# Optimization experiments

Hardware: AMD Instinct MI355X
Metric: run time of the kernel (lower is better)

Reference implementation:

```python
import jax, jax.numpy as jnp
import numpy as np

B, N, K = 32, 1024, 20

def _knn_idx(x, k):
    # x: [B, N, C] -> indices of k nearest neighbors (excluding self): [B, N, k]
    sq = jnp.sum(x * x, axis=-1)                      # [B, N]
    d = sq[:, :, None] + sq[:, None, :] - 2.0 * jnp.einsum('bnc,bmc->bnm', x, x)
    d = jnp.where(jnp.eye(x.shape[1], dtype=bool)[None], jnp.inf, d)
    _, idx = jax.lax.top_k(-d, k)                     # smallest distances
    return idx

def _edge_conv(x, k, mlp):
    # x: [B, N, C]; dynamic kNN graph + nn(cat[x_i, x_j - x_i]) + max over neighbors
    idx = _knn_idx(x, k)                              # [B, N, k]
    xj = jax.vmap(lambda xb, ib: xb[ib])(x, idx)      # [B, N, k, C]
    xi = jnp.broadcast_to(x[:, :, None, :], xj.shape)
    msg = mlp(jnp.concatenate([xi, xj - xi], axis=-1))  # [B, N, k, H]
    return jnp.max(msg, axis=2)                       # [B, N, H]

def setup_inputs() -> dict:
    key = jax.random.key(0)
    ks = jax.random.split(key, 16)
    def lin(kk, fi, fo):
        return jax.random.normal(kk, (fi, fo), dtype=jnp.float32) / np.sqrt(fi)
    x = jax.random.normal(ks[0], (B * N, 3), dtype=jnp.float32)
    batch = jnp.repeat(jnp.arange(B, dtype=jnp.int64), N)
    return {
        'x': x, 'batch': batch,
        'W1': lin(ks[1], 6, 64),   'b1': jnp.zeros((64,), jnp.float32),
        'W2': lin(ks[2], 64, 64),  'b2': jnp.zeros((64,), jnp.float32),
        'W3': lin(ks[3], 64, 64),  'b3': jnp.zeros((64,), jnp.float32),
        'W4': lin(ks[4], 128, 128),'b4': jnp.zeros((128,), jnp.float32),
        'Wp': lin(ks[5], 128, 512),'bp': jnp.zeros((512,), jnp.float32),
        'Wt1': lin(ks[6], 512, 256),'bt1': jnp.zeros((256,), jnp.float32),
        'Wt2': lin(ks[7], 256, 40), 'bt2': jnp.zeros((40,), jnp.float32),
    }

def reference(x, batch, W1, b1, W2, b2, W3, b3, W4, b4, Wp, bp, Wt1, bt1, Wt2, bt2):
    xb = x.reshape(B, N, -1)  # equal-sized clouds per batch vector
    mlp1 = lambda h: jax.nn.relu(jax.nn.relu(jax.nn.relu(h @ W1 + b1) @ W2 + b2) @ W3 + b3)
    mlp2 = lambda h: jax.nn.relu(h @ W4 + b4)
    out = _edge_conv(xb, K, mlp1)          # [B, N, 64]
    out = _edge_conv(out, K, mlp2)         # [B, N, 128]
    out = jax.nn.relu(out @ Wp + bp)       # [B, N, 512]
    out = jnp.max(out, axis=1)             # global max pool -> [B, 512]
    out = jax.nn.relu(out @ Wt1 + bt1) @ Wt2 + bt2  # [B, 40]
    return out
```

## Files before the change

### kernel.cpp

```cpp
#include <hip/hip_runtime.h>
#include <math.h>

#define BN   1024
#define NB   32
#define KNN  20
#define NROWS (NB*BN)

typedef __attribute__((ext_vector_type(8))) short bf16x8_t;
typedef __attribute__((ext_vector_type(4))) float f32x4_t;

__device__ __forceinline__ float finf() { return __builtin_huge_valf(); }

__device__ __forceinline__ unsigned short f2bf(float f) {
  union { float f; unsigned u; } v; v.f = f;
  unsigned r = v.u + 0x7FFFu + ((v.u >> 16) & 1u);
  return (unsigned short)(r >> 16);
}
__device__ __forceinline__ float bf2f(unsigned short h) {
  union { unsigned u; float f; } v; v.u = ((unsigned)h) << 16; return v.f;
}

__device__ __forceinline__ unsigned fkey(float d) {
  union { float f; unsigned u; } v; v.f = d;
  return (v.u & 0x80000000u) ? ~v.u : (v.u | 0x80000000u);
}

__device__ __forceinline__ void emit20(const unsigned (&kq)[16], unsigned thr,
                                       int lane, unsigned short* __restrict__ idx_out) {
  const unsigned long long lmask = (1ull << lane) - 1ull;
  int base = 0;
#pragma unroll
  for (int t = 0; t < 16; ++t) {
    const bool ok = (kq[t] <= thr);
    const unsigned long long m = __ballot(ok);
    if (ok) idx_out[base + (int)__popcll(m & lmask)] = (unsigned short)(kq[t] & 1023u);
    base += (int)__popcll(m);
  }
}

__device__ __forceinline__ void select20x2(const unsigned (&k0)[16], const unsigned (&k1)[16],
    int lane, unsigned short* __restrict__ o0, unsigned short* __restrict__ o1) {
  unsigned p0 = 0u, p1 = 0u;
  bool d0 = false, d1 = false;
#pragma unroll 1
  for (int b = 31; b >= 0; --b) {
    if (!d0) {
      const unsigned cand = p0 | (1u << b);
      int cnt = 0;
#pragma unroll
      for (int t = 0; t < 16; ++t) cnt += (int)__popcll(__ballot(k0[t] < cand));
      if (cnt == KNN)      { p0 = cand - 1u; d0 = true; }
      else if (cnt < KNN)  { p0 = cand; }
    }
    if (!d1) {
      const unsigned cand = p1 | (1u << b);
      int cnt = 0;
#pragma unroll
      for (int t = 0; t < 16; ++t) cnt += (int)__popcll(__ballot(k1[t] < cand));
      if (cnt == KNN)      { p1 = cand - 1u; d1 = true; }
      else if (cnt < KNN)  { p1 = cand; }
    }
    if (d0 && d1) break;
  }
  emit20(k0, p0, lane, o0);
  emit20(k1, p1, lane, o1);
}

__global__ __launch_bounds__(256) void prep_kernel(const float* __restrict__ W2, const float* __restrict__ W3,
    const float* __restrict__ W4, const float* __restrict__ Wp,
    unsigned short* __restrict__ w2b, unsigned short* __restrict__ w3b,
    unsigned short* __restrict__ w4b, unsigned short* __restrict__ wpb) {
  const int i = blockIdx.x * 256 + threadIdx.x;
  if (i < 512) {
    const int lane = i & 63, ks = (i >> 6) & 1, nt = i >> 7;
    const int col = nt*16 + (lane & 15), k0 = ks*32 + ((lane >> 4) << 3);
#pragma unroll
    for (int e = 0; e < 8; ++e) w2b[i*8 + e] = f2bf(W2[(size_t)(k0 + e)*64 + col]);
  } else if (i < 1024) {
    const int ii = i - 512;
    const int lane = ii & 63, ks = (ii >> 6) & 1, nt = ii >> 7;
    const int col = nt*16 + (lane & 15), k0 = ks*32 + ((lane >> 4) << 3);
#pragma unroll
    for (int e = 0; e < 8; ++e) w3b[ii*8 + e] = f2bf(W3[(size_t)(k0 + e)*64 + col]);
  } else if (i < 3072) {
    const int ii = i - 1024;
    const int lane = ii & 63, ks = (ii >> 6) & 3, nt = ii >> 8;
    const int col = nt*16 + (lane & 15), k0 = ks*32 + ((lane >> 4) << 3);
#pragma unroll
    for (int e = 0; e < 8; ++e) w4b[ii*8 + e] = f2bf(W4[(size_t)(k0 + e)*128 + col]);
  } else if (i < 11264) {
    const int ii = i - 3072;
    const int lane = ii & 63, ks = (ii >> 6) & 3, nt = ii >> 8;
    const int col = nt*16 + (lane & 15), k0 = ks*32 + ((lane >> 4) << 3);
#pragma unroll
    for (int e = 0; e < 8; ++e) {
      const float v = Wp[(size_t)(k0 + e)*512 + col];
      const unsigned short h = f2bf(v);
      wpb[ii*8 + e]         = h;
      wpb[65536 + ii*8 + e] = f2bf(v - bf2f(h));
    }
  }
}

__global__ __launch_bounds__(256) void knn3_kernel(const float* __restrict__ x, unsigned short* __restrict__ idxo) {
  const int pair = blockIdx.x * 4 + (threadIdx.x >> 6);
  const int lane = threadIdx.x & 63;
  const int row0 = pair * 2;
  const int b = row0 >> 10;
  const int ia = row0 & (BN - 1), ib = ia + 1;
  const float* xb = x + (size_t)b * BN * 3;
  const float xa0 = xb[ia*3+0], xa1 = xb[ia*3+1], xa2 = xb[ia*3+2];
  const float xb0 = xb[ib*3+0], xb1 = xb[ib*3+1], xb2 = xb[ib*3+2];
  const float sqa = xa0*xa0 + xa1*xa1 + xa2*xa2;
  const float sqb = xb0*xb0 + xb1*xb1 + xb2*xb2;
  unsigned k0[16], k1[16];
#pragma unroll
  for (int t = 0; t < 16; ++t) {
    const int j = (t << 6) | lane;
    const float a0 = xb[j*3+0], a1 = xb[j*3+1], a2 = xb[j*3+2];
    const float sqj = a0*a0 + a1*a1 + a2*a2;
    const float da  = sqa + sqj - 2.0f*(xa0*a0 + xa1*a1 + xa2*a2);
    const float db  = sqb + sqj - 2.0f*(xb0*a0 + xb1*a1 + xb2*a2);
    k0[t] = (j == ia) ? 0xFFFFFFFFu : ((fkey(da) & 0xFFFFFC00u) | (unsigned)j);
    k1[t] = (j == ib) ? 0xFFFFFFFFu : ((fkey(db) & 0xFFFFFC00u) | (unsigned)j);
  }
  select20x2(k0, k1, lane, idxo + (size_t)row0 * KNN, idxo + (size_t)(row0 + 1) * KNN);
}

__global__ __launch_bounds__(256) void edge1_mfma_kernel(const float* __restrict__ x, const unsigned short* __restrict__ idx,
    const float* __restrict__ W1, const float* __restrict__ B1,
    const unsigned short* __restrict__ w2b, const float* __restrict__ B2,
    const unsigned short* __restrict__ w3b, const float* __restrict__ B3,
    float* __restrict__ out1, unsigned short* __restrict__ hib,
    unsigned short* __restrict__ lob, float* __restrict__ sqbuf) {
  __shared__ unsigned short Hs1[80*64];
  __shared__ unsigned short Hs2[80*64];
  __shared__ float part[4][4];
  const int t = threadIdx.x, lane = t & 63, w = t >> 6;
  const int node0 = blockIdx.x * 4;

  const int bcol = w*16 + (lane & 15);
  bf16x8_t Bf2[2], Bf3[2];
#pragma unroll
  for (int ks = 0; ks < 2; ++ks) {
    Bf2[ks] = *(const bf16x8_t*)&w2b[(size_t)((w*2 + ks)*64 + lane) * 8];
    Bf3[ks] = *(const bf16x8_t*)&w3b[(size_t)((w*2 + ks)*64 + lane) * 8];
  }

  float w1c[6];
#pragma unroll
  for (int c = 0; c < 6; ++c) w1c[c] = W1[c*64 + lane];
  const float b1o = B1[lane];
  for (int r = w; r < 80; r += 4) {
    const int g = (r * 205) >> 12;
    const int e = r - g*20;
    const int node = node0 + g;
    const int b = node >> 10;
    const int j = idx[(size_t)node*KNN + e];
    const float xi0 = x[(size_t)node*3+0], xi1 = x[(size_t)node*3+1], xi2 = x[(size_t)node*3+2];
    const size_t jr = ((size_t)(b*BN + j))*3;
    const float h3 = x[jr+0]-xi0, h4 = x[jr+1]-xi1, h5 = x[jr+2]-xi2;
    float z = b1o + xi0*w1c[0] + xi1*w1c[1] + xi2*w1c[2]
                  + h3*w1c[3] + h4*w1c[4] + h5*w1c[5];
    z = fmaxf(z, 0.0f);
    Hs1[r*64 + (((lane>>3) ^ (r&7))<<3) + (lane&7)] = f2bf(z);
  }
  __syncthreads();

  f32x4_t acc[5];
#pragma unroll
  for (int mt = 0; mt < 5; ++mt) acc[mt] = (f32x4_t){0,0,0,0};
#pragma unroll
  for (int ks = 0; ks < 2; ++ks) {
#pragma unroll
    for (int mt = 0; mt < 5; ++mt) {
      const int r = mt*16 + (lane & 15);
      const int chunk = ks*4 + (lane >> 4);
      const bf16x8_t a = *(const bf16x8_t*)&Hs1[r*64 + ((chunk ^ (r&7))<<3)];
      acc[mt] = __builtin_amdgcn_mfma_f32_16x16x32_bf16(a, Bf2[ks], acc[mt], 0,0,0);
    }
  }
  {
    const float b2o = B2[bcol];
    const int rbase = (lane >> 4) * 4;
#pragma unroll
    for (int mt = 0; mt < 5; ++mt) {
#pragma unroll
      for (int reg = 0; reg < 4; ++reg) {
        const int row = mt*16 + rbase + reg;
        const float v = fmaxf(acc[mt][reg] + b2o, 0.0f);
        Hs2[row*64 + (((bcol>>3) ^ (row&7))<<3) + (bcol&7)] = f2bf(v);
      }
    }
  }
  __syncthreads();

#pragma unroll
  for (int mt = 0; mt < 5; ++mt) acc[mt] = (f32x4_t){0,0,0,0};
#pragma unroll
  for (int ks = 0; ks < 2; ++ks) {
#pragma unroll
    for (int mt = 0; mt < 5; ++mt) {
      const int r = mt*16 + (lane & 15);
      const int chunk = ks*4 + (lane >> 4);
      const bf16x8_t a = *(const bf16x8_t*)&Hs2[r*64 + ((chunk ^ (r&7))<<3)];
      acc[mt] = __builtin_amdgcn_mfma_f32_16x16x32_bf16(a, Bf3[ks], acc[mt], 0,0,0);
    }
  }

  {
    const float b3o = B3[bcol];
    const int rbase = (lane >> 4) * 4;
    float nm0 = 0.0f, nm1 = 0.0f, nm2 = 0.0f, nm3 = 0.0f;
#pragma unroll
    for (int mt = 0; mt < 5; ++mt) {
#pragma unroll
      for (int reg = 0; reg < 4; ++reg) {
        const int r = mt*16 + rbase + reg;
        const int g = (r * 205) >> 12;
        const float v = fmaxf(acc[mt][reg] + b3o, 0.0f);
        nm0 = (g == 0) ? fmaxf(nm0, v) : nm0;
        nm1 = (g == 1) ? fmaxf(nm1, v) : nm1;
        nm2 = (g == 2) ? fmaxf(nm2, v) : nm2;
        nm3 = (g == 3) ? fmaxf(nm3, v) : nm3;
      }
    }
#pragma unroll
    for (int off = 16; off <= 32; off <<= 1) {
      nm0 = fmaxf(nm0, __shfl_xor(nm0, off, 64));
      nm1 = fmaxf(nm1, __shfl_xor(nm1, off, 64));
      nm2 = fmaxf(nm2, __shfl_xor(nm2, off, 64));
      nm3 = fmaxf(nm3, __shfl_xor(nm3, off, 64));
    }
    const int gq = lane >> 4;
    const float m = (gq == 0) ? nm0 : (gq == 1) ? nm1 : (gq == 2) ? nm2 : nm3;
    const int node = node0 + gq;
    out1[(size_t)node*64 + bcol] = m;
    const unsigned short h = f2bf(m);
    hib[(size_t)node*64 + bcol] = h;
    lob[(size_t)node*64 + bcol] = f2bf(m - bf2f(h));
    float s = m * m;
#pragma unroll
    for (int off = 1; off <= 8; off <<= 1) s += __shfl_xor(s, off, 64);
    if ((lane & 15) == 0) part[gq][w] = s;
  }
  __syncthreads();
  if (t < 4) sqbuf[node0 + t] = part[t][0] + part[t][1] + part[t][2] + part[t][3];
}

__global__ __launch_bounds__(512) void knn64_mfma_kernel(
    const unsigned short* __restrict__ hi, const unsigned short* __restrict__ lo,
    const float* __restrict__ sq, unsigned short* __restrict__ idxo) {
  __shared__ unsigned Dmat[16 * 1024];
  const int t = threadIdx.x, lane = t & 63, w = t >> 6;
  const int i0  = blockIdx.x * 16;
  const int b   = i0 >> 10;
  const int i0l = i0 & (BN - 1);

  const size_t arow = (size_t)(i0 + (lane & 15)) * 64;
  const int    koff = (lane >> 4) * 8;
  bf16x8_t Ahi[2], Alo[2];
#pragma unroll
  for (int ks = 0; ks < 2; ++ks) {
    Ahi[ks] = *(const bf16x8_t*)&hi[arow + ks*32 + koff];
    Alo[ks] = *(const bf16x8_t*)&lo[arow + ks*32 + koff];
  }

  f32x4_t acc[8];
#pragma unroll
  for (int nt = 0; nt < 8; ++nt) {
    const int jl = (8*w + nt)*16 + (lane & 15);
    const size_t jrow = ((size_t)(b << 10) + jl) * 64;
    const bf16x8_t Bhi0 = *(const bf16x8_t*)&hi[jrow + koff];
    const bf16x8_t Bhi1 = *(const bf16x8_t*)&hi[jrow + 32 + koff];
    const bf16x8_t Blo0 = *(const bf16x8_t*)&lo[jrow + koff];
    const bf16x8_t Blo1 = *(const bf16x8_t*)&lo[jrow + 32 + koff];
    f32x4_t a = (f32x4_t){0,0,0,0};
    a = __builtin_amdgcn_mfma_f32_16x16x32_bf16(Ahi[0], Bhi0, a, 0,0,0);
    a = __builtin_amdgcn_mfma_f32_16x16x32_bf16(Ahi[1], Bhi1, a, 0,0,0);
    a = __builtin_amdgcn_mfma_f32_16x16x32_bf16(Ahi[0], Blo0, a, 0,0,0);
    a = __builtin_amdgcn_mfma_f32_16x16x32_bf16(Ahi[1], Blo1, a, 0,0,0);
    a = __builtin_amdgcn_mfma_f32_16x16x32_bf16(Alo[0], Bhi0, a, 0,0,0);
    a = __builtin_amdgcn_mfma_f32_16x16x32_bf16(Alo[1], Bhi1, a, 0,0,0);
    acc[nt] = a;
  }

  const int rbase = (lane >> 4) * 4;
  float sqr[4];
#pragma unroll
  for (int r = 0; r < 4; ++r) sqr[r] = sq[i0 + rbase + r];
#pragma unroll
  for (int nt = 0; nt < 8; ++nt) {
    const int jl = (8*w + nt)*16 + (lane & 15);
    const float sqj = sq[(b << 10) + jl];
#pragma unroll
    for (int r = 0; r < 4; ++r) {
      const float d = sqr[r] + sqj - 2.0f * acc[nt][r];
      const unsigned kq = (jl == i0l + rbase + r) ? 0xFFFFFFFFu
                        : ((fkey(d) & 0xFFFFFC00u) | (unsigned)jl);
      Dmat[(rbase + r)*1024 + jl] = kq;
    }
  }
  __syncthreads();

  const int r0 = 2*w, r1 = 2*w + 1;
  unsigned k0[16], k1[16];
#pragma unroll
  for (int tt = 0; tt < 16; ++tt) {
    k0[tt] = Dmat[r0*1024 + tt*64 + lane];
    k1[tt] = Dmat[r1*1024 + tt*64 + lane];
  }
  select20x2(k0, k1, lane, idxo + (size_t)(i0 + r0) * KNN, idxo + (size_t)(i0 + r1) * KNN);
}

__global__ __launch_bounds__(256) void edge2_mfma_kernel(const float* __restrict__ f, const unsigned short* __restrict__ idx,
    const unsigned short* __restrict__ w4b, const float* __restrict__ B4,
    unsigned short* __restrict__ o2hi, unsigned short* __restrict__ o2lo) {
  __shared__ unsigned short Hs[160*128];
  const int t = threadIdx.x, lane = t & 63, w = t >> 6;
  const int node0 = blockIdx.x * 8;

  bf16x8_t Bfrag[2][4];
#pragma unroll
  for (int nti = 0; nti < 2; ++nti)
#pragma unroll
    for (int ks = 0; ks < 4; ++ks)
      Bfrag[nti][ks] = *(const bf16x8_t*)&w4b[(size_t)(((2*w + nti)*4 + ks)*64 + lane) * 8];

  const int cq = (lane & 15) * 4;
  const int ch1 = cq >> 3, ch2 = 8 + (cq >> 3), sub = cq & 4;
#pragma unroll 2
  for (int i = 0; i < 10; ++i) {
    const int r = w*40 + i*4 + (lane >> 4);
    const int g = (r * 205) >> 12;
    const int e = r - g*20;
    const int node = node0 + g;
    const int b = node >> 10;
    const int j = idx[(size_t)node*KNN + e];
    const float4 xi = *(const float4*)&f[(size_t)node*64 + cq];
    const float4 xj = *(const float4*)&f[((size_t)(b*BN + j))*64 + cq];
    ushort4 hxi, hdf;
    hxi.x = f2bf(xi.x); hxi.y = f2bf(xi.y); hxi.z = f2bf(xi.z); hxi.w = f2bf(xi.w);
    hdf.x = f2bf(xj.x - xi.x); hdf.y = f2bf(xj.y - xi.y);
    hdf.z = f2bf(xj.z - xi.z); hdf.w = f2bf(xj.w - xi.w);
    *(ushort4*)&Hs[r*128 + ((ch1 ^ (r&7))<<3) + sub] = hxi;
    *(ushort4*)&Hs[r*128 + ((ch2 ^ (r&7))<<3) + sub] = hdf;
  }
  __syncthreads();

  f32x4_t acc[10][2];
#pragma unroll
  for (int mt = 0; mt < 10; ++mt) { acc[mt][0] = (f32x4_t){0,0,0,0}; acc[mt][1] = (f32x4_t){0,0,0,0}; }
#pragma unroll
  for (int ks = 0; ks < 4; ++ks) {
#pragma unroll
    for (int mt = 0; mt < 10; ++mt) {
      const int r = mt*16 + (lane & 15);
      const int chunk = ks*4 + (lane >> 4);
      const bf16x8_t a = *(const bf16x8_t*)&Hs[r*128 + ((chunk ^ (r&7))<<3)];
      acc[mt][0] = __builtin_amdgcn_mfma_f32_16x16x32_bf16(a, Bfrag[0][ks], acc[mt][0], 0,0,0);
      acc[mt][1] = __builtin_amdgcn_mfma_f32_16x16x32_bf16(a, Bfrag[1][ks], acc[mt][1], 0,0,0);
    }
  }

  const float bb0 = B4[(2*w+0)*16 + (lane & 15)];
  const float bb1 = B4[(2*w+1)*16 + (lane & 15)];
  const int rbase = (lane >> 4) * 4;
  float nm[8][2];
#pragma unroll
  for (int g = 0; g < 8; ++g) { nm[g][0] = 0.0f; nm[g][1] = 0.0f; }
#pragma unroll
  for (int mt = 0; mt < 10; ++mt) {
#pragma unroll
    for (int reg = 0; reg < 4; ++reg) {
      const int base = mt*16 + reg;
      const int glo = base / 20, ghi = (base + 12) / 20;
      const int r = base + rbase;
      const float v0 = fmaxf(acc[mt][0][reg] + bb0, 0.0f);
      const float v1 = fmaxf(acc[mt][1][reg] + bb1, 0.0f);
      if (glo == ghi) {
        nm[glo][0] = fmaxf(nm[glo][0], v0);
        nm[glo][1] = fmaxf(nm[glo][1], v1);
      } else {
        const bool hi = (r >= ghi*20);
        nm[glo][0] = hi ? nm[glo][0] : fmaxf(nm[glo][0], v0);
        nm[glo][1] = hi ? nm[glo][1] : fmaxf(nm[glo][1], v1);
        nm[ghi][0] = hi ? fmaxf(nm[ghi][0], v0) : nm[ghi][0];
        nm[ghi][1] = hi ? fmaxf(nm[ghi][1], v1) : nm[ghi][1];
      }
    }
  }
#pragma unroll
  for (int off = 16; off <= 32; off <<= 1)
#pragma unroll
    for (int g = 0; g < 8; ++g) {
      nm[g][0] = fmaxf(nm[g][0], __shfl_xor(nm[g][0], off, 64));
      nm[g][1] = fmaxf(nm[g][1], __shfl_xor(nm[g][1], off, 64));
    }
  const int gq = lane >> 4;
#pragma unroll
  for (int g = 0; g < 8; ++g) {
    if ((g & 3) == gq) {
#pragma unroll
      for (int nti = 0; nti < 2; ++nti) {
        const float m = nm[g][nti];
        const size_t o = (size_t)(node0 + g)*128 + (2*w + nti)*16 + (lane & 15);
        const unsigned short h = f2bf(m);
        o2hi[o] = h;
        o2lo[o] = f2bf(m - bf2f(h));
      }
    }
  }
}

__global__ __launch_bounds__(512) void pool_mfma_kernel(const unsigned short* __restrict__ o2hi,
    const unsigned short* __restrict__ o2lo, const unsigned short* __restrict__ wpb,
    const float* __restrict__ bp, float* __restrict__ pooled) {
  const int t = threadIdx.x, lane = t & 63, w = t >> 6;
  const int b = blockIdx.x >> 3, chunk = blockIdx.x & 7;
  const int row0 = b*BN + chunk*128;
  const int koff = (lane >> 4) * 8;
  bf16x8_t Bhi[4][4], Blo[4][4];
#pragma unroll
  for (int q = 0; q < 4; ++q)
#pragma unroll
    for (int ks = 0; ks < 4; ++ks) {
      const int nt = w*4 + q;
      Bhi[q][ks] = *(const bf16x8_t*)&wpb[(size_t)((nt*4 + ks)*64 + lane) * 8];
      Blo[q][ks] = *(const bf16x8_t*)&wpb[65536 + (size_t)((nt*4 + ks)*64 + lane) * 8];
    }
  float colmax[4] = {-finf(), -finf(), -finf(), -finf()};
#pragma unroll 2
  for (int mt = 0; mt < 8; ++mt) {
    const size_t ar = (size_t)(row0 + mt*16 + (lane & 15)) * 128;
    bf16x8_t Ahi[4], Alo[4];
#pragma unroll
    for (int ks = 0; ks < 4; ++ks) {
      Ahi[ks] = *(const bf16x8_t*)&o2hi[ar + ks*32 + koff];
      Alo[ks] = *(const bf16x8_t*)&o2lo[ar + ks*32 + koff];
    }
#pragma unroll
    for (int q = 0; q < 4; ++q) {
      f32x4_t a = (f32x4_t){0,0,0,0};
#pragma unroll
      for (int ks = 0; ks < 4; ++ks) {
        a = __builtin_amdgcn_mfma_f32_16x16x32_bf16(Ahi[ks], Bhi[q][ks], a, 0,0,0);
        a = __builtin_amdgcn_mfma_f32_16x16x32_bf16(Ahi[ks], Blo[q][ks], a, 0,0,0);
        a = __builtin_amdgcn_mfma_f32_16x16x32_bf16(Alo[ks], Bhi[q][ks], a, 0,0,0);
      }
#pragma unroll
      for (int reg = 0; reg < 4; ++reg) colmax[q] = fmaxf(colmax[q], a[reg]);
    }
  }
#pragma unroll
  for (int off = 16; off <= 32; off <<= 1)
#pragma unroll
    for (int q = 0; q < 4; ++q) colmax[q] = fmaxf(colmax[q], __shfl_xor(colmax[q], off, 64));
  if (lane < 16) {
#pragma unroll
    for (int q = 0; q < 4; ++q) {
      const int col = (w*4 + q)*16 + lane;
      const float m = fmaxf(colmax[q] + bp[col], 0.0f);
      atomicMax((int*)(pooled + (size_t)b*512 + col), __float_as_int(m));
    }
  }
}

__global__ __launch_bounds__(256) void head_kernel(const float* __restrict__ pooled,
    const float* __restrict__ Wt1, const float* __restrict__ bt1,
    const float* __restrict__ Wt2, const float* __restrict__ bt2,
    float* __restrict__ out) {
  __shared__ float psh[512];
  __shared__ float h1sh[256];
  const int t = threadIdx.x, b = blockIdx.x;
  psh[t]       = pooled[(size_t)b*512 + t];
  psh[t + 256] = pooled[(size_t)b*512 + t + 256];
  __syncthreads();
  float z = bt1[t];
  for (int j = 0; j < 512; ++j) z += psh[j] * Wt1[(size_t)j*256 + t];
  h1sh[t] = fmaxf(z, 0.0f);
  __syncthreads();
  if (t < 40) {
    float z2 = bt2[t];
    for (int j = 0; j < 256; ++j) z2 += h1sh[j] * Wt2[(size_t)j*40 + t];
    out[(size_t)b*40 + t] = z2;
  }
}

extern "C" void kernel_launch(void* const* d_in, const int* in_sizes, int n_in,
                              void* d_out, int out_size, void* d_ws, size_t ws_size,
                              hipStream_t stream) {
  const float* x   = (const float*)d_in[0];
  const float* W1  = (const float*)d_in[2];
  const float* B1  = (const float*)d_in[3];
  const float* W2  = (const float*)d_in[4];
  const float* B2  = (const float*)d_in[5];
  const float* W3  = (const float*)d_in[6];
  const float* B3  = (const float*)d_in[7];
  const float* W4  = (const float*)d_in[8];
  const float* B4  = (const float*)d_in[9];
  const float* Wp  = (const float*)d_in[10];
  const float* bp  = (const float*)d_in[11];
  const float* Wt1 = (const float*)d_in[12];
  const float* bt1 = (const float*)d_in[13];
  const float* Wt2 = (const float*)d_in[14];
  const float* bt2 = (const float*)d_in[15];
  float* out = (float*)d_out;

  char* ws = (char*)d_ws;
  const size_t OFF_SQ     = 0;
  const size_t OFF_IDX1   = 131072;
  const size_t OFF_OUT1   = 1441792;
  const size_t OFF_IDX2   = 9830400;
  const size_t OFF_X      = 11141120;
  const size_t OFF_POOLED = 27918336;
  const size_t OFF_W2B    = 27983872;
  const size_t OFF_W3B    = 27992064;
  const size_t OFF_W4B    = 28000256;
  const size_t OFF_WPB    = 28033024;
  const size_t WS_NEEDED  = 28295168;
  if (ws_size < WS_NEEDED) return;

  float*          sqbuf  = (float*)(ws + OFF_SQ);
  unsigned short* idx1   = (unsigned short*)(ws + OFF_IDX1);
  float*          out1   = (float*)(ws + OFF_OUT1);
  unsigned short* idx2   = (unsigned short*)(ws + OFF_IDX2);
  unsigned short* hib    = (unsigned short*)(ws + OFF_X);
  unsigned short* lob    = (unsigned short*)(ws + OFF_X + 4194304);
  unsigned short* o2hi   = (unsigned short*)(ws + OFF_X);
  unsigned short* o2lo   = (unsigned short*)(ws + OFF_X + 8388608);
  float*          pooled = (float*)(ws + OFF_POOLED);
  unsigned short* w2b    = (unsigned short*)(ws + OFF_W2B);
  unsigned short* w3b    = (unsigned short*)(ws + OFF_W3B);
  unsigned short* w4b    = (unsigned short*)(ws + OFF_W4B);
  unsigned short* wpb    = (unsigned short*)(ws + OFF_WPB);

  prep_kernel      <<<44,          256, 0, stream>>>(W2, W3, W4, Wp, w2b, w3b, w4b, wpb);
  knn3_kernel      <<<NROWS/8,     256, 0, stream>>>(x, idx1);
  edge1_mfma_kernel<<<NROWS/4,     256, 0, stream>>>(x, idx1, W1, B1, w2b, B2, w3b, B3,
                                                     out1, hib, lob, sqbuf);
  knn64_mfma_kernel<<<NROWS/16,    512, 0, stream>>>(hib, lob, sqbuf, idx2);
  edge2_mfma_kernel<<<NROWS/8,     256, 0, stream>>>(out1, idx2, w4b, B4, o2hi, o2lo);
  hipMemsetAsync(pooled, 0, NB*512*sizeof(float), stream);
  pool_mfma_kernel <<<NB*8,        512, 0, stream>>>(o2hi, o2lo, wpb, bp, pooled);
  head_kernel      <<<NB,          256, 0, stream>>>(pooled, Wt1, bt1, Wt2, bt2, out);
}
```

Baseline: 368.2 us.

## Shrink knn64 blocks to 8 rows and use fixed-depth radix select

The 64-dim kNN kernel now processes 8 query rows per 256-thread block instead of 16 per 512-thread block, which halves the shared distance matrix and walks column tiles in four chunks to reduce accumulator register pressure. Half of the MFMA output rows are wasted because the 16-row tile only has 8 valid rows. The top-20 radix select now runs over a fixed 22 high bits with no early exit, processes both rows in a lockstep loop, and breaks ties at the threshold bucket by rank. This is meant to raise occupancy and remove divergent early-exit control, but it doubles B-operand loads and MFMA work per useful output row.

```diff
diff --git a/kernel.cpp b/kernel.cpp
--- a/kernel.cpp
+++ b/kernel.cpp
@@ -25,45 +25,49 @@
   return (v.u & 0x80000000u) ? ~v.u : (v.u | 0x80000000u);
 }
 
-__device__ __forceinline__ void emit20(const unsigned (&kq)[16], unsigned thr,
-                                       int lane, unsigned short* __restrict__ idx_out) {
+__device__ __forceinline__ void emit20c(const unsigned (&kq)[16], unsigned P, int cnt_lt,
+                                        int lane, unsigned short* __restrict__ idx_out) {
   const unsigned long long lmask = (1ull << lane) - 1ull;
-  int base = 0;
+  const int need = KNN - cnt_lt;
+  int base_lt = 0, base_eq = 0;
 #pragma unroll
   for (int t = 0; t < 16; ++t) {
-    const bool ok = (kq[t] <= thr);
-    const unsigned long long m = __ballot(ok);
-    if (ok) idx_out[base + (int)__popcll(m & lmask)] = (unsigned short)(kq[t] & 1023u);
-    base += (int)__popcll(m);
+    const bool lt = (kq[t] < P);
+    const bool eq = ((kq[t] - P) < 1024u);
+    const unsigned long long mlt = __ballot(lt);
+    const unsigned long long meq = __ballot(eq);
+    if (lt) idx_out[base_lt + (int)__popcll(mlt & lmask)] = (unsigned short)(kq[t] & 1023u);
+    const int erank = base_eq + (int)__popcll(meq & lmask);
+    if (eq && erank < need) idx_out[cnt_lt + erank] = (unsigned short)(kq[t] & 1023u);
+    base_lt += (int)__popcll(mlt);
+    base_eq += (int)__popcll(meq);
   }
 }
 
 __device__ __forceinline__ void select20x2(const unsigned (&k0)[16], const unsigned (&k1)[16],
     int lane, unsigned short* __restrict__ o0, unsigned short* __restrict__ o1) {
   unsigned p0 = 0u, p1 = 0u;
-  bool d0 = false, d1 = false;
 #pragma unroll 1
-  for (int b = 31; b >= 0; --b) {
-    if (!d0) {
-      const unsigned cand = p0 | (1u << b);
-      int cnt = 0;
-#pragma unroll
-      for (int t = 0; t < 16; ++t) cnt += (int)__popcll(__ballot(k0[t] < cand));
-      if (cnt == KNN)      { p0 = cand - 1u; d0 = true; }
-      else if (cnt < KNN)  { p0 = cand; }
-    }
-    if (!d1) {
-      const unsigned cand = p1 | (1u << b);
-      int cnt = 0;
-#pragma unroll
-      for (int t = 0; t < 16; ++t) cnt += (int)__popcll(__ballot(k1[t] < cand));
-      if (cnt == KNN)      { p1 = cand - 1u; d1 = true; }
-      else if (cnt < KNN)  { p1 = cand; }
-    }
-    if (d0 && d1) break;
-  }
-  emit20(k0, p0, lane, o0);
-  emit20(k1, p1, lane, o1);
+  for (int b = 31; b >= 10; --b) {
+    const unsigned c0 = p0 | (1u << b);
+    const unsigned c1 = p1 | (1u << b);
+    int n0 = 0, n1 = 0;
+#pragma unroll
+    for (int t = 0; t < 16; ++t) {
+      n0 += (int)__popcll(__ballot(k0[t] < c0));
+      n1 += (int)__popcll(__ballot(k1[t] < c1));
+    }
+    if (n0 < KNN) p0 = c0;
+    if (n1 < KNN) p1 = c1;
+  }
+  int c0n = 0, c1n = 0;
+#pragma unroll
+  for (int t = 0; t < 16; ++t) {
+    c0n += (int)__popcll(__ballot(k0[t] < p0));
+    c1n += (int)__popcll(__ballot(k1[t] < p1));
+  }
+  emit20c(k0, p0, c0n, lane, o0);
+  emit20c(k1, p1, c1n, lane, o1);
 }
 
 __global__ __launch_bounds__(256) void prep_kernel(const float* __restrict__ W2, const float* __restrict__ W3,
@@ -248,17 +252,18 @@
   if (t < 4) sqbuf[node0 + t] = part[t][0] + part[t][1] + part[t][2] + part[t][3];
 }
 
-__global__ __launch_bounds__(512) void knn64_mfma_kernel(
+__global__ __launch_bounds__(256) void knn64_mfma_kernel(
     const unsigned short* __restrict__ hi, const unsigned short* __restrict__ lo,
     const float* __restrict__ sq, unsigned short* __restrict__ idxo) {
-  __shared__ unsigned Dmat[16 * 1024];
+  __shared__ unsigned Dmat[8 * 1024];
   const int t = threadIdx.x, lane = t & 63, w = t >> 6;
-  const int i0  = blockIdx.x * 16;
+  const int i0  = blockIdx.x * 8;
   const int b   = i0 >> 10;
   const int i0l = i0 & (BN - 1);
 
-  const size_t arow = (size_t)(i0 + (lane & 15)) * 64;
-  const int    koff = (lane >> 4) * 8;
+  const int arow_i = min(i0 + (lane & 15), NROWS - 1);
+  const size_t arow = (size_t)arow_i * 64;
+  const int koff = (lane >> 4) * 8;
   bf16x8_t Ahi[2], Alo[2];
 #pragma unroll
   for (int ks = 0; ks < 2; ++ks) {
@@ -266,39 +271,44 @@
     Alo[ks] = *(const bf16x8_t*)&lo[arow + ks*32 + koff];
   }
 
-  f32x4_t acc[8];
-#pragma unroll
-  for (int nt = 0; nt < 8; ++nt) {
-    const int jl = (8*w + nt)*16 + (lane & 15);
-    const size_t jrow = ((size_t)(b << 10) + jl) * 64;
-    const bf16x8_t Bhi0 = *(const bf16x8_t*)&hi[jrow + koff];
-    const bf16x8_t Bhi1 = *(const bf16x8_t*)&hi[jrow + 32 + koff];
-    const bf16x8_t Blo0 = *(const bf16x8_t*)&lo[jrow + koff];
-    const bf16x8_t Blo1 = *(const bf16x8_t*)&lo[jrow + 32 + koff];
-    f32x4_t a = (f32x4_t){0,0,0,0};
-    a = __builtin_amdgcn_mfma_f32_16x16x32_bf16(Ahi[0], Bhi0, a, 0,0,0);
-    a = __builtin_amdgcn_mfma_f32_16x16x32_bf16(Ahi[1], Bhi1, a, 0,0,0);
-    a = __builtin_amdgcn_mfma_f32_16x16x32_bf16(Ahi[0], Blo0, a, 0,0,0);
-    a = __builtin_amdgcn_mfma_f32_16x16x32_bf16(Ahi[1], Blo1, a, 0,0,0);
-    a = __builtin_amdgcn_mfma_f32_16x16x32_bf16(Alo[0], Bhi0, a, 0,0,0);
-    a = __builtin_amdgcn_mfma_f32_16x16x32_bf16(Alo[1], Bhi1, a, 0,0,0);
-    acc[nt] = a;
-  }
-
   const int rbase = (lane >> 4) * 4;
   float sqr[4];
 #pragma unroll
-  for (int r = 0; r < 4; ++r) sqr[r] = sq[i0 + rbase + r];
-#pragma unroll
-  for (int nt = 0; nt < 8; ++nt) {
-    const int jl = (8*w + nt)*16 + (lane & 15);
-    const float sqj = sq[(b << 10) + jl];
-#pragma unroll
-    for (int r = 0; r < 4; ++r) {
-      const float d = sqr[r] + sqj - 2.0f * acc[nt][r];
-      const unsigned kq = (jl == i0l + rbase + r) ? 0xFFFFFFFFu
-                        : ((fkey(d) & 0xFFFFFC00u) | (unsigned)jl);
-      Dmat[(rbase + r)*1024 + jl] = kq;
+  for (int r = 0; r < 4; ++r) sqr[r] = sq[min(i0 + rbase + r, NROWS - 1)];
+
+#pragma unroll 1
+  for (int h = 0; h < 4; ++h) {
+    f32x4_t acc[4];
+#pragma unroll
+    for (int nt = 0; nt < 4; ++nt) {
+      const int jl = (w*16 + h*4 + nt)*16 + (lane & 15);
+      const size_t jrow = ((size_t)(b << 10) + jl) * 64;
+      const bf16x8_t Bhi0 = *(const bf16x8_t*)&hi[jrow + koff];
+      const bf16x8_t Bhi1 = *(const bf16x8_t*)&hi[jrow + 32 + koff];
+      const bf16x8_t Blo0 = *(const bf16x8_t*)&lo[jrow + koff];
+      const bf16x8_t Blo1 = *(const bf16x8_t*)&lo[jrow + 32 + koff];
+      f32x4_t a = (f32x4_t){0,0,0,0};
+      a = __builtin_amdgcn_mfma_f32_16x16x32_bf16(Ahi[0], Bhi0, a, 0,0,0);
+      a = __builtin_amdgcn_mfma_f32_16x16x32_bf16(Ahi[1], Bhi1, a, 0,0,0);
+      a = __builtin_amdgcn_mfma_f32_16x16x32_bf16(Ahi[0], Blo0, a, 0,0,0);
+      a = __builtin_amdgcn_mfma_f32_16x16x32_bf16(Ahi[1], Blo1, a, 0,0,0);
+      a = __builtin_amdgcn_mfma_f32_16x16x32_bf16(Alo[0], Bhi0, a, 0,0,0);
+      a = __builtin_amdgcn_mfma_f32_16x16x32_bf16(Alo[1], Bhi1, a, 0,0,0);
+      acc[nt] = a;
+    }
+    if (rbase < 8) {
+#pragma unroll
+      for (int nt = 0; nt < 4; ++nt) {
+        const int jl = (w*16 + h*4 + nt)*16 + (lane & 15);
+        const float sqj = sq[(b << 10) + jl];
+#pragma unroll
+        for (int r = 0; r < 4; ++r) {
+          const float d = sqr[r] + sqj - 2.0f * acc[nt][r];
+          const unsigned kq = (jl == i0l + rbase + r) ? 0xFFFFFFFFu
+                            : ((fkey(d) & 0xFFFFFC00u) | (unsigned)jl);
+          Dmat[(rbase + r)*1024 + jl] = kq;
+        }
+      }
     }
   }
   __syncthreads();
@@ -539,7 +549,7 @@
   knn3_kernel      <<<NROWS/8,     256, 0, stream>>>(x, idx1);
   edge1_mfma_kernel<<<NROWS/4,     256, 0, stream>>>(x, idx1, W1, B1, w2b, B2, w3b, B3,
                                                      out1, hib, lob, sqbuf);
-  knn64_mfma_kernel<<<NROWS/16,    512, 0, stream>>>(hib, lob, sqbuf, idx2);
+  knn64_mfma_kernel<<<NROWS/8,     256, 0, stream>>>(hib, lob, sqbuf, idx2);
   edge2_mfma_kernel<<<NROWS/8,     256, 0, stream>>>(out1, idx2, w4b, B4, o2hi, o2lo);
   hipMemsetAsync(pooled, 0, NB*512*sizeof(float), stream);
   pool_mfma_kernel <<<NB*8,        512, 0, stream>>>(o2hi, o2lo, wpb, bp, pooled);
```

Result: slower. 429.0 us (+16.5%).
